# Kernel optimization log

Measured on AMD Instinct MI355X. Metric: run time of the kernel, lower is better.

The kernel has to match this reference:

```python
import jax, jax.numpy as jnp
import numpy as np

NUM_HEADS = 12
DROP = 0.5


def setup_inputs() -> dict:
    key = jax.random.key(0)
    k1, k2, k3, k4 = jax.random.split(key, 4)
    B, N, C = 64, 577, 768
    x = jax.random.normal(k1, (B, N, C), dtype=jnp.float32)
    mask = jax.random.uniform(k2, (B, NUM_HEADS, N - 1), dtype=jnp.float32)
    Wqkv = jax.random.normal(k3, (C, 3 * C), dtype=jnp.float32) * 0.02
    bqkv = jnp.zeros((3 * C,), dtype=jnp.float32)
    Wproj = jax.random.normal(k4, (C, C), dtype=jnp.float32) * 0.02
    bproj = jnp.zeros((C,), dtype=jnp.float32)
    return {"x": x, "mask": mask, "Wqkv": Wqkv, "bqkv": bqkv,
            "Wproj": Wproj, "bproj": bproj}


def _drop_tokens(t, idx):
    # t: [B,H,N,D]; keep CLS token, gather sorted random indices from the rest
    rest = jnp.take_along_axis(t[:, :, 1:, :], idx[..., None], axis=2)
    return jnp.concatenate([t[:, :, :1, :], rest], axis=2)


def reference(x, mask, Wqkv, bqkv, Wproj, bproj):
    B, N, C = x.shape
    H = NUM_HEADS
    D = C // H
    scale = D ** -0.5
    target_len = N - int(N * DROP)  # kept tokens incl. CLS

    qkv = (x @ Wqkv + bqkv).reshape(B, N, 3, H, D)
    qkv = jnp.transpose(qkv, (2, 0, 3, 1, 4))  # [3,B,H,N,D]
    q, k, v = qkv[0], qkv[1], qkv[2]

    # random token drop (rand branch): topk of random mask, sort indices
    _, idx = jax.lax.top_k(mask, target_len - 1)  # [B,H,target_len-1]
    idx = jnp.sort(idx, axis=-1)
    k_p = _drop_tokens(k, idx)  # [B,H,target_len,D]
    v_p = _drop_tokens(v, idx)

    attn = jax.nn.softmax(
        jnp.einsum('bhnd,bhmd->bhnm', q, k_p) * scale, axis=-1)
    out = jnp.einsum('bhnm,bhmd->bhnd', attn, v_p)
    out = jnp.transpose(out, (0, 2, 1, 3)).reshape(B, N, C)
    return out @ Wproj + bproj
```

## Files before the change

kernel.cpp:

```cpp
#include <hip/hip_runtime.h>
#include <stdint.h>

#define B_      64
#define N_TOK   577
#define C_      768
#define H_      12
#define BH_     768
#define M_ROWS  36928
#define M_PAD   36992
#define KEEP    289
#define KP      320

typedef __attribute__((ext_vector_type(8))) short   bf16x8;
typedef __attribute__((ext_vector_type(4))) float   floatx4;
typedef __attribute__((ext_vector_type(4))) short   short4v;

static __device__ __forceinline__ unsigned short f2bf(float f) {
  union { float f; unsigned u; } a; a.f = f;
  unsigned u = a.u;
  u = u + 0x7FFFu + ((u >> 16) & 1u);
  return (unsigned short)(u >> 16);
}

static __device__ __forceinline__ void gl_lds16(const void* g, void* l) {
  __builtin_amdgcn_global_load_lds(
      (const __attribute__((address_space(1))) void*)g,
      (__attribute__((address_space(3))) void*)l, 16, 0, 0);
}

__global__ void topk_kernel(const float* __restrict__ mask, int* __restrict__ pos) {
  __shared__ float vals[576];
  __shared__ int woff[9];
  int row = blockIdx.x;
  int t = threadIdx.x;
  float v = mask[(size_t)row * 576 + t];
  vals[t] = v;
  __syncthreads();
  int rank = 0;
  for (int j = 0; j < 576; ++j) {
    float u = vals[j];
    rank += ((u > v) || (u == v && j < t)) ? 1 : 0;
  }
  bool sel = rank < (KEEP - 1);
  unsigned long long ball = __ballot(sel ? 1 : 0);
  int lane = t & 63, w = t >> 6;
  int lp = __popcll(ball & ((1ull << lane) - 1ull));
  if (lane == 0) woff[w] = __popcll(ball);
  __syncthreads();
  int base = 0;
  for (int i = 0; i < w; ++i) base += woff[i];
  pos[(size_t)row * 577 + 1 + t] = sel ? (1 + base + lp) : -1;
  if (t == 0) pos[(size_t)row * 577] = 0;
}

__global__ void convx_kernel(const float* __restrict__ x, unsigned short* __restrict__ xb) {
  size_t i = ((size_t)blockIdx.x * 256 + threadIdx.x) * 4;
  short4v o;
  if (i < (size_t)M_ROWS * C_) {
    float4 v = *(const float4*)(x + i);
    o.x = (short)f2bf(v.x); o.y = (short)f2bf(v.y);
    o.z = (short)f2bf(v.z); o.w = (short)f2bf(v.w);
  } else {
    o.x = 0; o.y = 0; o.z = 0; o.w = 0;
  }
  *(short4v*)(xb + i) = o;
}

__global__ void convwT_kernel(const float* __restrict__ W, unsigned short* __restrict__ Wt,
                              int N) {
  __shared__ unsigned short tile[64 * 72];
  int n0 = blockIdx.x * 64, k0 = blockIdx.y * 64;
  int t = threadIdx.x;
  for (int p = 0; p < 4; ++p) {
    int s = p * 256 + t;
    int k = s >> 4, nc = s & 15;
    float4 v = *(const float4*)(W + (size_t)(k0 + k) * N + n0 + nc * 4);
    short4v o;
    o.x = (short)f2bf(v.x); o.y = (short)f2bf(v.y);
    o.z = (short)f2bf(v.z); o.w = (short)f2bf(v.w);
    *(short4v*)(tile + k * 72 + nc * 4) = o;
  }
  __syncthreads();
  for (int p = 0; p < 2; ++p) {
    int s = p * 256 + t;
    int n = s >> 3, kc = s & 7;
    bf16x8 o;
    for (int j = 0; j < 8; ++j) o[j] = (short)tile[(kc * 8 + j) * 72 + n];
    *(bf16x8*)(Wt + (size_t)(n0 + n) * 768 + k0 + kc * 8) = o;
  }
}

__global__ void zeropad_kernel(unsigned short* __restrict__ Kp, unsigned short* __restrict__ Vp) {
  size_t idx = (size_t)blockIdx.x * 256 + threadIdx.x;
  int bh = (int)(idx / (31 * 64));
  int rem = (int)(idx % (31 * 64));
  int r = KEEP + rem / 64, d = rem & 63;
  size_t o = ((size_t)bh * KP + r) * 64 + d;
  Kp[o] = 0; Vp[o] = 0;
}

__global__ __launch_bounds__(256) void qkv_gemm_kernel(
    const unsigned short* __restrict__ A, const unsigned short* __restrict__ Bt,
    const float* __restrict__ bias, const int* __restrict__ pos,
    unsigned short* __restrict__ Q, unsigned short* __restrict__ Kp,
    unsigned short* __restrict__ Vp) {
  __shared__ unsigned short As[128 * 64];
  __shared__ unsigned short Bs[128 * 64];
  const int tid = threadIdx.x;
  const int lane = tid & 63, wv = tid >> 6;
  const int quad = lane >> 4, lcol = lane & 15;
  const int wm = wv & 1, wn = wv >> 1;
  int sid = blockIdx.x;
  int m_t, n_t;
  if (sid < 5184) {
    int sb = sid / 48, r = sid % 48;
    int gm = sb % 36, gn = sb / 36;
    m_t = gm * 8 + (r & 7);
    n_t = gn * 6 + (r >> 3);
  } else { m_t = 288; n_t = sid - 5184; }
  const int m0 = m_t * 128, n0 = n_t * 128;
  const int swz = lcol & 7;

  floatx4 acc[4][4] = {};
  for (int k0 = 0; k0 < 768; k0 += 64) {
#pragma unroll
    for (int c = 0; c < 4; ++c) {
      int s = c * 256 + tid;
      int r = s >> 3, cs = s & 7;
      int gc = ((cs ^ (r & 7)) << 3);
      gl_lds16(A  + (size_t)(m0 + r) * 768 + k0 + gc, As + s * 8);
      gl_lds16(Bt + (size_t)(n0 + r) * 768 + k0 + gc, Bs + s * 8);
    }
    __syncthreads();
#pragma unroll
    for (int kh = 0; kh < 2; ++kh) {
      bf16x8 af[4], bfr[4];
      int cc = kh * 4 + quad;
#pragma unroll
      for (int i = 0; i < 4; ++i)
        af[i] = *(const bf16x8*)(As + (wm * 64 + i * 16 + lcol) * 64 + ((cc ^ swz) << 3));
#pragma unroll
      for (int i = 0; i < 4; ++i)
        bfr[i] = *(const bf16x8*)(Bs + (wn * 64 + i * 16 + lcol) * 64 + ((cc ^ swz) << 3));
#pragma unroll
      for (int i = 0; i < 4; ++i)
#pragma unroll
        for (int j = 0; j < 4; ++j)
          acc[i][j] = __builtin_amdgcn_mfma_f32_16x16x32_bf16(af[i], bfr[j], acc[i][j], 0, 0, 0);
    }
    __syncthreads();
  }
  const int nbase = n0 + wn * 64;
  const int which = nbase / 768;
  const int h = (nbase - which * 768) >> 6;
  float bv[4];
#pragma unroll
  for (int nt = 0; nt < 4; ++nt) bv[nt] = bias[nbase + nt * 16 + lcol];
#pragma unroll
  for (int mt = 0; mt < 4; ++mt) {
#pragma unroll
    for (int r = 0; r < 4; ++r) {
      int m = m0 + wm * 64 + mt * 16 + quad * 4 + r;
      if (m >= M_ROWS) continue;
      int b = m / 577, t = m - b * 577;
      int bh = b * 12 + h;
      if (which == 0) {
        size_t base = ((size_t)bh * 577 + t) * 64;
#pragma unroll
        for (int nt = 0; nt < 4; ++nt)
          Q[base + nt * 16 + lcol] = f2bf(acc[mt][nt][r] + bv[nt]);
      } else {
        int p = pos[(size_t)bh * 577 + t];
        if (p >= 0) {
          size_t base = ((size_t)bh * KP + p) * 64;
          if (which == 1) {
            int sw = p & 7;
#pragma unroll
            for (int nt = 0; nt < 4; ++nt) {
              int d = nt * 16 + lcol;
              int d2 = (d & 7) | (((d >> 3) ^ sw) << 3);
              Kp[base + d2] = f2bf(acc[mt][nt][r] + bv[nt]);
            }
          } else {
#pragma unroll
            for (int nt = 0; nt < 4; ++nt)
              Vp[base + nt * 16 + lcol] = f2bf(acc[mt][nt][r] + bv[nt]);
          }
        }
      }
    }
  }
}

__global__ void transv_kernel(const unsigned short* __restrict__ Vp,
                              unsigned short* __restrict__ VpT) {
  __shared__ unsigned short tile[64 * 72];
  int bh = blockIdx.y, p0 = blockIdx.x * 64;
  int t = threadIdx.x;
  for (int pp = 0; pp < 2; ++pp) {
    int s = pp * 256 + t;
    int p = s >> 3, dc = s & 7;
    bf16x8 v = *(const bf16x8*)(Vp + ((size_t)bh * KP + p0 + p) * 64 + dc * 8);
    *(bf16x8*)(tile + p * 72 + dc * 8) = v;
  }
  __syncthreads();
  for (int pp = 0; pp < 2; ++pp) {
    int s = pp * 256 + t;
    int d = s >> 3, pc = s & 7;
    bf16x8 o;
    for (int j = 0; j < 8; ++j) o[j] = (short)tile[(pc * 8 + j) * 72 + d];
    *(bf16x8*)(VpT + ((size_t)bh * 64 + d) * KP + p0 + pc * 8) = o;
  }
}

__global__ __launch_bounds__(256) void attn_kernel(
    const unsigned short* __restrict__ Q, const unsigned short* __restrict__ Kp,
    const unsigned short* __restrict__ VpT, unsigned short* __restrict__ attnout) {
  __shared__ unsigned short S[320 * 64];
  const int tid = threadIdx.x;
  const int lane = tid & 63, w = tid >> 6;
  const int quad = lane >> 4, lcol = lane & 15;
  const int g = blockIdx.x;
  const int chunk = g / 80, within = g - chunk * 80;
  const int by = chunk * 8 + (within & 7);
  const int bx = within >> 3;
  const int q0 = bx * 64 + w * 16;

  const unsigned short* kg = Kp + (size_t)by * KP * 64;
#pragma unroll
  for (int c = 0; c < 10; ++c) {
    int s = c * 256 + tid;
    gl_lds16(kg + s * 8, S + s * 8);
  }

  bf16x8 aq[2];
  {
    int qr = q0 + lcol;
    if (qr < N_TOK) {
      const unsigned short* qp = Q + ((size_t)by * N_TOK + qr) * 64;
      aq[0] = *(const bf16x8*)(qp + quad * 8);
      aq[1] = *(const bf16x8*)(qp + 32 + quad * 8);
    } else {
      bf16x8 z = {0, 0, 0, 0, 0, 0, 0, 0};
      aq[0] = z; aq[1] = z;
    }
  }
  __syncthreads();

  floatx4 sacc[20] = {};
  __builtin_amdgcn_s_setprio(1);
#pragma unroll
  for (int nt = 0; nt < 19; ++nt) {
    int r16 = nt * 16 + lcol;
    const unsigned short* kb = S + r16 * 64;
    int sw = r16 & 7;
    bf16x8 b0 = *(const bf16x8*)(kb + ((quad ^ sw) << 3));
    bf16x8 b1 = *(const bf16x8*)(kb + (((quad + 4) ^ sw) << 3));
    sacc[nt] = __builtin_amdgcn_mfma_f32_16x16x32_bf16(aq[0], b0, sacc[nt], 0, 0, 0);
    sacc[nt] = __builtin_amdgcn_mfma_f32_16x16x32_bf16(aq[1], b1, sacc[nt], 0, 0, 0);
  }
  __builtin_amdgcn_s_setprio(0);

  const float scale = 0.125f;
  float inva[4];
  for (int r = 0; r < 4; ++r) {
    float mx = -1e30f;
#pragma unroll
    for (int nt = 0; nt < 20; ++nt) {
      int n = nt * 16 + lcol;
      float s = sacc[nt][r] * scale;
      if (n < KEEP) mx = fmaxf(mx, s);
    }
    for (int off = 1; off < 16; off <<= 1) mx = fmaxf(mx, __shfl_xor(mx, off, 64));
    float sum = 0.f;
#pragma unroll
    for (int nt = 0; nt < 20; ++nt) {
      int n = nt * 16 + lcol;
      float e = (n < KEEP) ? __expf(sacc[nt][r] * scale - mx) : 0.f;
      sacc[nt][r] = e;
      sum += e;
    }
    for (int off = 1; off < 16; off <<= 1) sum += __shfl_xor(sum, off, 64);
    inva[r] = 1.f / sum;
  }
  __syncthreads();

#pragma unroll
  for (int r = 0; r < 4; ++r) {
    int rowl = w * 16 + quad * 4 + r;
    int swp = rowl & 7;
#pragma unroll
    for (int nt = 0; nt < 20; ++nt) {
      int n = nt * 16 + lcol;
      int u = n >> 3;
      int u2 = (u & 0x38) | ((u & 7) ^ swp);
      S[rowl * 320 + u2 * 8 + (n & 7)] = f2bf(sacc[nt][r] * inva[r]);
    }
  }
  __syncthreads();

  floatx4 oacc[4] = {};
  const int prow = w * 16 + lcol;
  const int psw = prow & 7;
  __builtin_amdgcn_s_setprio(1);
#pragma unroll
  for (int kc = 0; kc < 10; ++kc) {
    int u = kc * 4 + quad;
    int u2 = (u & 0x38) | ((u & 7) ^ psw);
    bf16x8 pa = *(const bf16x8*)(S + prow * 320 + u2 * 8);
#pragma unroll
    for (int nt = 0; nt < 4; ++nt) {
      bf16x8 vb = *(const bf16x8*)(VpT + ((size_t)by * 64 + nt * 16 + lcol) * KP + kc * 32 + quad * 8);
      oacc[nt] = __builtin_amdgcn_mfma_f32_16x16x32_bf16(pa, vb, oacc[nt], 0, 0, 0);
    }
  }
  __builtin_amdgcn_s_setprio(0);

  int b = by / H_, h = by - b * H_;
#pragma unroll
  for (int nt = 0; nt < 4; ++nt)
#pragma unroll
    for (int r = 0; r < 4; ++r) {
      int qr = bx * 64 + w * 16 + quad * 4 + r;
      if (qr < N_TOK)
        attnout[((size_t)(b * N_TOK + qr)) * C_ + h * 64 + nt * 16 + lcol] = f2bf(oacc[nt][r]);
    }
}

__global__ __launch_bounds__(256) void proj_gemm_kernel(
    const unsigned short* __restrict__ A, const unsigned short* __restrict__ Bt,
    const float* __restrict__ bias, float* __restrict__ out) {
  __shared__ unsigned short As[128 * 64];
  __shared__ unsigned short Bs[128 * 64];
  const int tid = threadIdx.x;
  const int lane = tid & 63, wv = tid >> 6;
  const int quad = lane >> 4, lcol = lane & 15;
  const int wm = wv & 1, wn = wv >> 1;
  int sid = blockIdx.x;
  int m_t, n_t;
  if (sid < 1728) {
    int sb = sid / 48, r = sid % 48;
    m_t = sb * 8 + (r & 7);
    n_t = r >> 3;
  } else { m_t = 288; n_t = sid - 1728; }
  const int m0 = m_t * 128, n0 = n_t * 128;
  const int swz = lcol & 7;

  floatx4 acc[4][4] = {};
  for (int k0 = 0; k0 < 768; k0 += 64) {
#pragma unroll
    for (int c = 0; c < 4; ++c) {
      int s = c * 256 + tid;
      int r = s >> 3, cs = s & 7;
      int gc = ((cs ^ (r & 7)) << 3);
      gl_lds16(A  + (size_t)(m0 + r) * 768 + k0 + gc, As + s * 8);
      gl_lds16(Bt + (size_t)(n0 + r) * 768 + k0 + gc, Bs + s * 8);
    }
    __syncthreads();
#pragma unroll
    for (int kh = 0; kh < 2; ++kh) {
      bf16x8 af[4], bfr[4];
      int cc = kh * 4 + quad;
#pragma unroll
      for (int i = 0; i < 4; ++i)
        af[i] = *(const bf16x8*)(As + (wm * 64 + i * 16 + lcol) * 64 + ((cc ^ swz) << 3));
#pragma unroll
      for (int i = 0; i < 4; ++i)
        bfr[i] = *(const bf16x8*)(Bs + (wn * 64 + i * 16 + lcol) * 64 + ((cc ^ swz) << 3));
#pragma unroll
      for (int i = 0; i < 4; ++i)
#pragma unroll
        for (int j = 0; j < 4; ++j)
          acc[i][j] = __builtin_amdgcn_mfma_f32_16x16x32_bf16(af[i], bfr[j], acc[i][j], 0, 0, 0);
    }
    __syncthreads();
  }
  const int nbase = n0 + wn * 64;
  float bv[4];
#pragma unroll
  for (int nt = 0; nt < 4; ++nt) bv[nt] = bias[nbase + nt * 16 + lcol];
#pragma unroll
  for (int mt = 0; mt < 4; ++mt)
#pragma unroll
    for (int r = 0; r < 4; ++r) {
      int m = m0 + wm * 64 + mt * 16 + quad * 4 + r;
      if (m >= M_ROWS) continue;
#pragma unroll
      for (int nt = 0; nt < 4; ++nt)
        out[(size_t)m * C_ + nbase + nt * 16 + lcol] = acc[mt][nt][r] + bv[nt];
    }
}

extern "C" void kernel_launch(void* const* d_in, const int* in_sizes, int n_in,
                              void* d_out, int out_size, void* d_ws, size_t ws_size,
                              hipStream_t stream) {
  const float* x     = (const float*)d_in[0];
  const float* mask  = (const float*)d_in[1];
  const float* Wqkv  = (const float*)d_in[2];
  const float* bqkv  = (const float*)d_in[3];
  const float* Wproj = (const float*)d_in[4];
  const float* bproj = (const float*)d_in[5];
  float* out = (float*)d_out;

  char* ws = (char*)d_ws;
  unsigned short* xb     = (unsigned short*)(ws);
  unsigned short* attno  = xb;
  unsigned short* WqkvT  = (unsigned short*)(ws + 56819712);
  unsigned short* WprojT = (unsigned short*)(ws + 60358656);
  int*            pos    = (int*)(ws + 61538304);
  unsigned short* Qb     = (unsigned short*)(ws + 63310848);
  unsigned short* Kpb    = (unsigned short*)(ws + 120032256);
  unsigned short* Vpb    = (unsigned short*)(ws + 151489536);
  unsigned short* VpTb   = (unsigned short*)(ws + 182946816);

  hipLaunchKernelGGL(topk_kernel,     dim3(768),      dim3(576), 0, stream, mask, pos);
  hipLaunchKernelGGL(convx_kernel,    dim3(27744),    dim3(256), 0, stream, x, xb);
  hipLaunchKernelGGL(convwT_kernel,   dim3(36, 12),   dim3(256), 0, stream, Wqkv, WqkvT, 2304);
  hipLaunchKernelGGL(convwT_kernel,   dim3(12, 12),   dim3(256), 0, stream, Wproj, WprojT, 768);
  hipLaunchKernelGGL(zeropad_kernel,  dim3(5952),     dim3(256), 0, stream, Kpb, Vpb);
  hipLaunchKernelGGL(qkv_gemm_kernel, dim3(5202),     dim3(256), 0, stream, xb, WqkvT, bqkv, pos, Qb, Kpb, Vpb);
  hipLaunchKernelGGL(transv_kernel,   dim3(5, 768),   dim3(256), 0, stream, Vpb, VpTb);
  hipLaunchKernelGGL(attn_kernel,     dim3(7680),     dim3(256), 0, stream, Qb, Kpb, VpTb, attno);
  hipLaunchKernelGGL(proj_gemm_kernel,dim3(1734),     dim3(256), 0, stream, attno, WprojT, bproj, out);
}
```

Before: 734.9 us.

## Double-buffer LDS in QKV and projection GEMMs with interleaved prefetch

Both GEMM kernels now share a core that double-buffers the A and B tiles in LDS. Global-to-LDS loads for the next k-tiles are issued in pieces between groups of MFMAs, with explicit vmcnt waits, barriers and priority bumps. The goal is to hide global load latency behind matrix math, where the old loop stalled on __syncthreads around each load. In exchange it doubles LDS use per block, which may lower occupancy, and relies on fragile hand-written waitcnt accounting.

```diff
diff --git a/kernel.cpp b/kernel.cpp
--- a/kernel.cpp
+++ b/kernel.cpp
@@ -99,13 +99,95 @@
   Kp[o] = 0; Vp[o] = 0;
 }
 
+static __device__ __forceinline__ void stage_half(const unsigned short* src,
+                                                  unsigned short* lds, int tid) {
+#pragma unroll
+  for (int c = 0; c < 2; ++c) {
+    int s = c * 256 + tid;
+    int r = s >> 3, cs = s & 7;
+    int gc = (cs ^ (r & 7)) << 3;
+    gl_lds16(src + (size_t)r * 768 + gc, lds + s * 8);
+  }
+}
+
+static __device__ __forceinline__ void gemm8_core(
+    const unsigned short* __restrict__ A, const unsigned short* __restrict__ Bt,
+    int m0, int n0, int tid, unsigned short* As, unsigned short* Bs,
+    floatx4 (&acc)[4][4]) {
+  const int lane = tid & 63, wv = tid >> 6;
+  const int quad = lane >> 4, lcol = lane & 15;
+  const int wm = wv & 1, wn = wv >> 1;
+  const int swz = lcol & 7;
+
+#define STG_A(kt, half) stage_half(A  + (size_t)(m0 + 64*(half)) * 768 + (kt)*64, \
+                                   As + ((kt)&1)*8192 + (half)*4096, tid)
+#define STG_B(kt, half) stage_half(Bt + (size_t)(n0 + 64*(half)) * 768 + (kt)*64, \
+                                   Bs + ((kt)&1)*8192 + (half)*4096, tid)
+
+  STG_A(0, 0); STG_A(0, 1); STG_B(0, 0); STG_B(0, 1);
+  STG_A(1, 0); STG_A(1, 1); STG_B(1, 0);
+  asm volatile("s_waitcnt vmcnt(6)" ::: "memory");
+  __builtin_amdgcn_s_barrier();
+
+  for (int t = 0; t < 12; ++t) {
+    const unsigned short* Asl = As + (t & 1) * 8192;
+    const unsigned short* Bsl = Bs + (t & 1) * 8192;
+
+    bf16x8 af[4][2], bfr[4][2];
+#pragma unroll
+    for (int i = 0; i < 4; ++i)
+#pragma unroll
+      for (int ks = 0; ks < 2; ++ks) {
+        int cc = ks * 4 + quad;
+        af[i][ks]  = *(const bf16x8*)(Asl + (wm * 64 + i * 16 + lcol) * 64 + ((cc ^ swz) << 3));
+        bfr[i][ks] = *(const bf16x8*)(Bsl + (wn * 64 + i * 16 + lcol) * 64 + ((cc ^ swz) << 3));
+      }
+    if (t + 1 < 12) STG_B(t + 1, 1);
+    asm volatile("s_waitcnt lgkmcnt(0)" ::: "memory");
+    __builtin_amdgcn_sched_barrier(0);
+    __builtin_amdgcn_s_barrier();
+    __builtin_amdgcn_s_setprio(1);
+#pragma unroll
+    for (int j = 0; j < 4; ++j)
+#pragma unroll
+      for (int ks = 0; ks < 2; ++ks)
+        acc[0][j] = __builtin_amdgcn_mfma_f32_16x16x32_bf16(af[0][ks], bfr[j][ks], acc[0][j], 0, 0, 0);
+    __builtin_amdgcn_s_setprio(0);
+    __builtin_amdgcn_s_barrier();
+
+#pragma unroll
+    for (int p = 1; p < 4; ++p) {
+      if (t + 2 < 12) {
+        if (p == 1)      STG_A(t + 2, 0);
+        else if (p == 2) STG_A(t + 2, 1);
+        else             STG_B(t + 2, 0);
+      }
+      __builtin_amdgcn_s_barrier();
+      __builtin_amdgcn_s_setprio(1);
+#pragma unroll
+      for (int j = 0; j < 4; ++j)
+#pragma unroll
+        for (int ks = 0; ks < 2; ++ks)
+          acc[p][j] = __builtin_amdgcn_mfma_f32_16x16x32_bf16(af[p][ks], bfr[j][ks], acc[p][j], 0, 0, 0);
+      __builtin_amdgcn_s_setprio(0);
+      if (p == 3) {
+        if (t < 10)       asm volatile("s_waitcnt vmcnt(6)" ::: "memory");
+        else if (t == 10) asm volatile("s_waitcnt vmcnt(0)" ::: "memory");
+      }
+      __builtin_amdgcn_s_barrier();
+    }
+  }
+#undef STG_A
+#undef STG_B
+}
+
 __global__ __launch_bounds__(256) void qkv_gemm_kernel(
     const unsigned short* __restrict__ A, const unsigned short* __restrict__ Bt,
     const float* __restrict__ bias, const int* __restrict__ pos,
     unsigned short* __restrict__ Q, unsigned short* __restrict__ Kp,
     unsigned short* __restrict__ Vp) {
-  __shared__ unsigned short As[128 * 64];
-  __shared__ unsigned short Bs[128 * 64];
+  __shared__ unsigned short As[2 * 8192];
+  __shared__ unsigned short Bs[2 * 8192];
   const int tid = threadIdx.x;
   const int lane = tid & 63, wv = tid >> 6;
   const int quad = lane >> 4, lcol = lane & 15;
@@ -119,37 +201,10 @@
     n_t = gn * 6 + (r >> 3);
   } else { m_t = 288; n_t = sid - 5184; }
   const int m0 = m_t * 128, n0 = n_t * 128;
-  const int swz = lcol & 7;
 
   floatx4 acc[4][4] = {};
-  for (int k0 = 0; k0 < 768; k0 += 64) {
-#pragma unroll
-    for (int c = 0; c < 4; ++c) {
-      int s = c * 256 + tid;
-      int r = s >> 3, cs = s & 7;
-      int gc = ((cs ^ (r & 7)) << 3);
-      gl_lds16(A  + (size_t)(m0 + r) * 768 + k0 + gc, As + s * 8);
-      gl_lds16(Bt + (size_t)(n0 + r) * 768 + k0 + gc, Bs + s * 8);
-    }
-    __syncthreads();
-#pragma unroll
-    for (int kh = 0; kh < 2; ++kh) {
-      bf16x8 af[4], bfr[4];
-      int cc = kh * 4 + quad;
-#pragma unroll
-      for (int i = 0; i < 4; ++i)
-        af[i] = *(const bf16x8*)(As + (wm * 64 + i * 16 + lcol) * 64 + ((cc ^ swz) << 3));
-#pragma unroll
-      for (int i = 0; i < 4; ++i)
-        bfr[i] = *(const bf16x8*)(Bs + (wn * 64 + i * 16 + lcol) * 64 + ((cc ^ swz) << 3));
-#pragma unroll
-      for (int i = 0; i < 4; ++i)
-#pragma unroll
-        for (int j = 0; j < 4; ++j)
-          acc[i][j] = __builtin_amdgcn_mfma_f32_16x16x32_bf16(af[i], bfr[j], acc[i][j], 0, 0, 0);
-    }
-    __syncthreads();
-  }
+  gemm8_core(A, Bt, m0, n0, tid, As, Bs, acc);
+
   const int nbase = n0 + wn * 64;
   const int which = nbase / 768;
   const int h = (nbase - which * 768) >> 6;
@@ -330,8 +385,8 @@
 __global__ __launch_bounds__(256) void proj_gemm_kernel(
     const unsigned short* __restrict__ A, const unsigned short* __restrict__ Bt,
     const float* __restrict__ bias, float* __restrict__ out) {
-  __shared__ unsigned short As[128 * 64];
-  __shared__ unsigned short Bs[128 * 64];
+  __shared__ unsigned short As[2 * 8192];
+  __shared__ unsigned short Bs[2 * 8192];
   const int tid = threadIdx.x;
   const int lane = tid & 63, wv = tid >> 6;
   const int quad = lane >> 4, lcol = lane & 15;
@@ -344,37 +399,10 @@
     n_t = r >> 3;
   } else { m_t = 288; n_t = sid - 1728; }
   const int m0 = m_t * 128, n0 = n_t * 128;
-  const int swz = lcol & 7;
 
   floatx4 acc[4][4] = {};
-  for (int k0 = 0; k0 < 768; k0 += 64) {
-#pragma unroll
-    for (int c = 0; c < 4; ++c) {
-      int s = c * 256 + tid;
-      int r = s >> 3, cs = s & 7;
-      int gc = ((cs ^ (r & 7)) << 3);
-      gl_lds16(A  + (size_t)(m0 + r) * 768 + k0 + gc, As + s * 8);
-      gl_lds16(Bt + (size_t)(n0 + r) * 768 + k0 + gc, Bs + s * 8);
-    }
-    __syncthreads();
-#pragma unroll
-    for (int kh = 0; kh < 2; ++kh) {
-      bf16x8 af[4], bfr[4];
-      int cc = kh * 4 + quad;
-#pragma unroll
-      for (int i = 0; i < 4; ++i)
-        af[i] = *(const bf16x8*)(As + (wm * 64 + i * 16 + lcol) * 64 + ((cc ^ swz) << 3));
-#pragma unroll
-      for (int i = 0; i < 4; ++i)
-        bfr[i] = *(const bf16x8*)(Bs + (wn * 64 + i * 16 + lcol) * 64 + ((cc ^ swz) << 3));
-#pragma unroll
-      for (int i = 0; i < 4; ++i)
-#pragma unroll
-        for (int j = 0; j < 4; ++j)
-          acc[i][j] = __builtin_amdgcn_mfma_f32_16x16x32_bf16(af[i], bfr[j], acc[i][j], 0, 0, 0);
-    }
-    __syncthreads();
-  }
+  gemm8_core(A, Bt, m0, n0, tid, As, Bs, acc);
+
   const int nbase = n0 + wn * 64;
   float bv[4];
 #pragma unroll
```

After: 686.3 us. 1.07x faster.
